# Kernel optimization log

Hardware: AMD Instinct MI355X
Metric: run time of the kernel (lower is better)

The kernel has to match this reference:

```python
import jax, jax.numpy as jnp
import numpy as np

B, S, D = 32, 2048, 128


def setup_inputs() -> dict:
    key = jax.random.key(0)
    kq, kk, kv, km = jax.random.split(key, 4)
    queries = jax.random.normal(kq, (B, S, D), dtype=jnp.float32)
    keys = jax.random.normal(kk, (B, S, D), dtype=jnp.float32)
    values = jax.random.normal(kv, (B, S, D), dtype=jnp.float32)
    attention_mask = jax.random.randint(km, (B, S, S), 0, 2, dtype=jnp.int32)
    return {"queries": queries, "keys": keys, "values": values,
            "attention_mask": attention_mask}


def reference(queries, keys, values, attention_mask):
    d = queries.shape[-1]
    # scores: [B, S, S]
    scores = jnp.einsum("bqd,bkd->bqk", queries, keys) / jnp.sqrt(
        jnp.asarray(d, queries.dtype))
    scores = jnp.where(attention_mask == 0, jnp.asarray(-1e6, scores.dtype), scores)
    attn = jax.nn.softmax(scores, axis=-1)
    # dropout prob is 0.0 (eval-equivalent), so no dropout applied
    return jnp.einsum("bqk,bkd->bqd", attn, values)
```

## Files before the change

kernel.cpp:

```cpp
#include <hip/hip_runtime.h>

#define B_ 32
#define S_ 2048
#define D_ 128

typedef __bf16 bf16;
typedef __attribute__((ext_vector_type(8))) __bf16 bf16x8;
typedef __attribute__((ext_vector_type(16))) float f32x16;

__device__ __forceinline__ f32x16 mfma32(bf16x8 a, bf16x8 b, f32x16 c) {
  return __builtin_amdgcn_mfma_f32_32x32x16_bf16(a, b, c, 0, 0, 0);
}

__device__ __forceinline__ unsigned pk2(bf16 a, bf16 b) {
  unsigned short ua = __builtin_bit_cast(unsigned short, a);
  unsigned short ub = __builtin_bit_cast(unsigned short, b);
  return (unsigned)ua | ((unsigned)ub << 16);
}

__global__ __launch_bounds__(256) void vt_prepass(const float* __restrict__ V,
                                                  bf16* __restrict__ vthi,
                                                  bf16* __restrict__ vtlo) {
  const int bid = blockIdx.x;
  const int b = bid >> 5;
  const int kt = bid & 31;
  const int kbase = kt * 64;
  const int t = threadIdx.x;

  __shared__ __align__(16) bf16 Thi[128][66];
  __shared__ __align__(16) bf16 Tlo[128][66];

  {
    const int dc = t & 31;
    const int kr0 = t >> 5;
#pragma unroll
    for (int i = 0; i < 8; ++i) {
      const int kr = kr0 + i * 8;
      const float* src = V + ((size_t)b * S_ + kbase + kr) * D_ + dc * 4;
      float4 v = *(const float4*)src;
      float f[4] = {v.x, v.y, v.z, v.w};
#pragma unroll
      for (int j = 0; j < 4; ++j) {
        bf16 hi = (bf16)f[j];
        Thi[dc * 4 + j][kr] = hi;
        Tlo[dc * 4 + j][kr] = (bf16)(f[j] - (float)hi);
      }
    }
  }
  __syncthreads();
  {
    const int d = t >> 1;
    const int part = t & 1;
    const bf16(*Tp)[66] = part ? Tlo : Thi;
    bf16* dst = part ? vtlo : vthi;
    const unsigned* row = (const unsigned*)(&Tp[d][0]);
    unsigned wbuf[32];
#pragma unroll
    for (int i = 0; i < 32; ++i) wbuf[i] = row[i];
    const size_t rowbase = ((size_t)b * D_ + d) * S_ + kbase;
#pragma unroll
    for (int j = 0; j < 8; ++j) {
      const int jj = j ^ (d & 7);
      uint4 val;
      val.x = wbuf[4 * j + 0];
      val.y = wbuf[4 * j + 1];
      val.z = wbuf[4 * j + 2];
      val.w = wbuf[4 * j + 3];
      *(uint4*)(dst + rowbase + jj * 8) = val;
    }
  }
}

__global__ __launch_bounds__(256, 2) void attn_kernel(
    const float* __restrict__ Q, const float* __restrict__ K,
    const int* __restrict__ M, const bf16* __restrict__ vthi_g,
    const bf16* __restrict__ vtlo_g, float* __restrict__ Out) {
  extern __shared__ char smem[];
  unsigned* MaskW = (unsigned*)(smem + 65536);

  const int t = threadIdx.x;
  const int w = t >> 6;
  const int i31 = t & 31;
  const int h = (t >> 5) & 1;

  const int bid = blockIdx.x;
  const int xcd = bid & 7;
  const int slot = bid >> 3;
  const int b = xcd * 4 + (slot >> 4);
  const int qt = slot & 15;
  const int qbase = qt * 128;

  const int qrow = qbase + w * 32 + i31;
  const float* qsrc = Q + ((size_t)b * S_ + qrow) * D_;
  const float sc = 0.08838834764831843f;
  bf16x8 qh[8], ql[8];
#pragma unroll
  for (int ds = 0; ds < 8; ++ds) {
    const int d0 = ds * 16 + h * 8;
    float4 a = *(const float4*)(qsrc + d0);
    float4 c = *(const float4*)(qsrc + d0 + 4);
    float f[8] = {a.x, a.y, a.z, a.w, c.x, c.y, c.z, c.w};
#pragma unroll
    for (int e = 0; e < 8; ++e) {
      float v = f[e] * sc;
      bf16 hi = (bf16)v;
      qh[ds][e] = hi;
      ql[ds][e] = (bf16)(v - (float)hi);
    }
  }

  f32x16 acc[4];
#pragma unroll
  for (int dt = 0; dt < 4; ++dt)
#pragma unroll
    for (int e = 0; e < 16; ++e) acc[dt][e] = 0.f;
  float m_run = -3.0e38f, l_run = 0.f;

  const int qloc = w * 32 + i31;
  const unsigned qsw = (unsigned)(qloc & 15);

  for (int kt = 0; kt < 32; ++kt) {
    const int kbase = kt * 64;
    __syncthreads();

    {
      const int kr = t >> 2;
      const int db = (t & 3) * 32;
      const float* src = K + ((size_t)b * S_ + kbase + kr) * D_ + db;
      const unsigned rowb = (unsigned)kr << 8;
      const unsigned sw = (unsigned)(kr & 7) << 4;
#pragma unroll
      for (int j = 0; j < 4; ++j) {
        float4 a = *(const float4*)(src + j * 8);
        float4 c = *(const float4*)(src + j * 8 + 4);
        float f[8] = {a.x, a.y, a.z, a.w, c.x, c.y, c.z, c.w};
        bf16x8 hi8, lo8;
#pragma unroll
        for (int e = 0; e < 8; ++e) {
          bf16 hi = (bf16)f[e];
          hi8[e] = hi;
          lo8[e] = (bf16)(f[e] - (float)hi);
        }
        const unsigned off = rowb + (((unsigned)((db + 8 * j) * 2)) ^ sw);
        *(bf16x8*)(smem + off) = hi8;
        *(bf16x8*)(smem + 16384 + off) = lo8;
      }
    }
    {
      const int q = t >> 1;
      const int kb = (t & 1) * 8;
      const int* src = M + ((size_t)b * S_ + qbase + q) * S_ + kbase + kb * 4;
      const unsigned qs = (unsigned)(q & 15);
#pragma unroll
      for (int i = 0; i < 8; ++i) {
        int4 mm = *(const int4*)(src + i * 4);
        unsigned packed = (unsigned)(mm.x & 1) | ((unsigned)(mm.y & 1) << 8) |
                          ((unsigned)(mm.z & 1) << 16) |
                          ((unsigned)(mm.w & 1) << 24);
        MaskW[(unsigned)q * 16 + (((unsigned)(kb + i)) ^ qs)] = packed;
      }
    }
    {
#pragma unroll
      for (int u = 0; u < 4; ++u) {
        const int off = u * 4096 + t * 16;
        const int d = off >> 7;
        const int bk = (off >> 4) & 7;
        const size_t g = ((size_t)b * D_ + d) * S_ + kbase + bk * 8;
        *(bf16x8*)(smem + 32768 + off) = *(const bf16x8*)(vthi_g + g);
        *(bf16x8*)(smem + 49152 + off) = *(const bf16x8*)(vtlo_g + g);
      }
    }
    __syncthreads();

    f32x16 s[2];
#pragma unroll
    for (int ct = 0; ct < 2; ++ct)
#pragma unroll
      for (int e = 0; e < 16; ++e) s[ct][e] = 0.f;
#pragma unroll
    for (int ct = 0; ct < 2; ++ct) {
      const unsigned rowb = (unsigned)(ct * 32 + i31) << 8;
      const unsigned sw = (unsigned)(i31 & 7) << 4;
#pragma unroll
      for (int ds = 0; ds < 8; ++ds) {
        const unsigned off = rowb + (((unsigned)(ds * 32 + h * 16)) ^ sw);
        bf16x8 kh = *(const bf16x8*)(smem + off);
        bf16x8 kl = *(const bf16x8*)(smem + 16384 + off);
        s[ct] = mfma32(kh, qh[ds], s[ct]);
        s[ct] = mfma32(kl, qh[ds], s[ct]);
        s[ct] = mfma32(kh, ql[ds], s[ct]);
      }
    }

#pragma unroll
    for (int ct = 0; ct < 2; ++ct) {
#pragma unroll
      for (int rr = 0; rr < 4; ++rr) {
        const unsigned k4 = (unsigned)(ct * 8 + rr * 2 + h);
        const unsigned mm = MaskW[(unsigned)qloc * 16 + (k4 ^ qsw)];
#pragma unroll
        for (int rb = 0; rb < 4; ++rb) {
          const int r = rr * 4 + rb;
          s[ct][r] = ((mm >> (rb * 8)) & 1u) ? s[ct][r] : -1.0e6f;
        }
      }
    }

    float mx = -3.0e38f;
#pragma unroll
    for (int ct = 0; ct < 2; ++ct)
#pragma unroll
      for (int r = 0; r < 16; ++r) mx = fmaxf(mx, s[ct][r]);
    mx = fmaxf(mx, __shfl_xor(mx, 32, 64));
    const float m_new = fmaxf(m_run, mx);
    const float alpha = __expf(m_run - m_new);
    float rs = 0.f;
#pragma unroll
    for (int ct = 0; ct < 2; ++ct)
#pragma unroll
      for (int r = 0; r < 16; ++r) {
        const float p = __expf(s[ct][r] - m_new);
        s[ct][r] = p;
        rs += p;
      }
    rs += __shfl_xor(rs, 32, 64);
    l_run = l_run * alpha + rs;
    m_run = m_new;
#pragma unroll
    for (int dt = 0; dt < 4; ++dt) acc[dt] = acc[dt] * alpha;

#pragma unroll
    for (int ks = 0; ks < 4; ++ks) {
      const int ct = ks >> 1;
      const int a0 = (ks & 1) * 8;
      unsigned PKh[4], PKl[4];
#pragma unroll
      for (int y = 0; y < 4; ++y) {
        const float p0 = s[ct][a0 + 2 * y];
        const float p1 = s[ct][a0 + 2 * y + 1];
        bf16 h0 = (bf16)p0, h1 = (bf16)p1;
        PKh[y] = pk2(h0, h1);
        PKl[y] = pk2((bf16)(p0 - (float)h0), (bf16)(p1 - (float)h1));
      }
      const unsigned s0h = h ? PKh[0] : PKh[2];
      const unsigned s1h = h ? PKh[1] : PKh[3];
      const unsigned s0l = h ? PKl[0] : PKl[2];
      const unsigned s1l = h ? PKl[1] : PKl[3];
      const unsigned r0h = __shfl_xor(s0h, 32, 64);
      const unsigned r1h = __shfl_xor(s1h, 32, 64);
      const unsigned r0l = __shfl_xor(s0l, 32, 64);
      const unsigned r1l = __shfl_xor(s1l, 32, 64);
      uint4 fh, fl;
      fh.x = h ? r0h : PKh[0];
      fh.y = h ? r1h : PKh[1];
      fh.z = h ? PKh[2] : r0h;
      fh.w = h ? PKh[3] : r1h;
      fl.x = h ? r0l : PKl[0];
      fl.y = h ? r1l : PKl[1];
      fl.z = h ? PKl[2] : r0l;
      fl.w = h ? PKl[3] : r1l;
      bf16x8 pah = __builtin_bit_cast(bf16x8, fh);
      bf16x8 pal = __builtin_bit_cast(bf16x8, fl);
#pragma unroll
      for (int dt = 0; dt < 4; ++dt) {
        const unsigned d = (unsigned)(dt * 32 + i31);
        const unsigned off = d * 128 + ((((unsigned)(ks * 2 + h)) ^ (d & 7)) * 16);
        bf16x8 vh = *(const bf16x8*)(smem + 32768 + off);
        bf16x8 vl = *(const bf16x8*)(smem + 49152 + off);
        acc[dt] = mfma32(vh, pah, acc[dt]);
        acc[dt] = mfma32(vh, pal, acc[dt]);
        acc[dt] = mfma32(vl, pah, acc[dt]);
      }
    }
  }

  const float inv_l = 1.0f / l_run;
  float* orow = Out + ((size_t)b * S_ + qbase + w * 32 + i31) * D_;
#pragma unroll
  for (int dt = 0; dt < 4; ++dt) {
#pragma unroll
    for (int rr = 0; rr < 4; ++rr) {
      float4 o;
      o.x = acc[dt][rr * 4 + 0] * inv_l;
      o.y = acc[dt][rr * 4 + 1] * inv_l;
      o.z = acc[dt][rr * 4 + 2] * inv_l;
      o.w = acc[dt][rr * 4 + 3] * inv_l;
      *(float4*)(orow + dt * 32 + rr * 8 + h * 4) = o;
    }
  }
}

extern "C" void kernel_launch(void* const* d_in, const int* in_sizes, int n_in,
                              void* d_out, int out_size, void* d_ws,
                              size_t ws_size, hipStream_t stream) {
  (void)in_sizes; (void)n_in; (void)out_size; (void)ws_size;
  const float* Q = (const float*)d_in[0];
  const float* K = (const float*)d_in[1];
  const float* V = (const float*)d_in[2];
  const int* M = (const int*)d_in[3];
  float* Out = (float*)d_out;

  bf16* vthi = (bf16*)d_ws;
  bf16* vtlo = vthi + (size_t)B_ * D_ * S_;

  static int attr_set = 0;
  if (!attr_set) {
    hipFuncSetAttribute((const void*)attn_kernel,
                        hipFuncAttributeMaxDynamicSharedMemorySize, 73728);
    attr_set = 1;
  }

  vt_prepass<<<dim3(B_ * (S_ / 64)), dim3(256), 0, stream>>>(V, vthi, vtlo);
  attn_kernel<<<dim3(512), dim3(256), 73728, stream>>>(Q, K, M, vthi, vtlo, Out);
}
```

Before: 991.5 us.

## Double-buffer K/V tiles, prepack mask to bits, 256-row query blocks with exp2

Adds a separate mask_pack kernel that turns the int32 mask into 64-bit ballot words, so the attention kernel reads one u64 per row per tile instead of streaming int4 mask data. The attention kernel now uses 512 threads with 256 query rows per block and double-buffers K and V in 128KB of LDS, prefetching the next tile into registers while computing the current one. It also folds log2(e) into the Q scale and uses exp2, applies the mask by zeroing p after the exponent, and raises wave priority around the MFMA sections. The V prepass writes a tile-contiguous layout through a packed hi/lo LDS transpose. Costs include an extra kernel launch, larger LDS and register use, and a change in semantics for fully masked rows (l=0 instead of a uniform softmax).

```diff
diff --git a/kernel.cpp b/kernel.cpp
--- a/kernel.cpp
+++ b/kernel.cpp
@@ -3,8 +3,12 @@
 #define B_ 32
 #define S_ 2048
 #define D_ 128
+#define NT 32
+#define QB 256
 
 typedef __bf16 bf16;
+typedef unsigned u32;
+typedef unsigned long long u64;
 typedef __attribute__((ext_vector_type(8))) __bf16 bf16x8;
 typedef __attribute__((ext_vector_type(16))) float f32x16;
 
@@ -12,100 +16,142 @@
   return __builtin_amdgcn_mfma_f32_32x32x16_bf16(a, b, c, 0, 0, 0);
 }
 
-__device__ __forceinline__ unsigned pk2(bf16 a, bf16 b) {
+__device__ __forceinline__ u32 pk2(bf16 a, bf16 b) {
   unsigned short ua = __builtin_bit_cast(unsigned short, a);
   unsigned short ub = __builtin_bit_cast(unsigned short, b);
-  return (unsigned)ua | ((unsigned)ub << 16);
+  return (u32)ua | ((u32)ub << 16);
 }
 
 __global__ __launch_bounds__(256) void vt_prepass(const float* __restrict__ V,
                                                   bf16* __restrict__ vthi,
                                                   bf16* __restrict__ vtlo) {
   const int bid = blockIdx.x;
-  const int b = bid >> 5;
-  const int kt = bid & 31;
+  const int b = bid >> 5, kt = bid & 31;
   const int kbase = kt * 64;
   const int t = threadIdx.x;
-
-  __shared__ __align__(16) bf16 Thi[128][66];
-  __shared__ __align__(16) bf16 Tlo[128][66];
+  __shared__ u32 Tpk[128][67];
 
   {
-    const int dc = t & 31;
-    const int kr0 = t >> 5;
+    const int dc = t & 31, kr0 = t >> 5;
 #pragma unroll
     for (int i = 0; i < 8; ++i) {
       const int kr = kr0 + i * 8;
-      const float* src = V + ((size_t)b * S_ + kbase + kr) * D_ + dc * 4;
-      float4 v = *(const float4*)src;
+      float4 v = *(const float4*)(V + ((size_t)b * S_ + kbase + kr) * D_ + dc * 4);
       float f[4] = {v.x, v.y, v.z, v.w};
 #pragma unroll
       for (int j = 0; j < 4; ++j) {
         bf16 hi = (bf16)f[j];
-        Thi[dc * 4 + j][kr] = hi;
-        Tlo[dc * 4 + j][kr] = (bf16)(f[j] - (float)hi);
+        bf16 lo = (bf16)(f[j] - (float)hi);
+        Tpk[dc * 4 + j][kr] = pk2(hi, lo);
       }
     }
   }
   __syncthreads();
-  {
-    const int d = t >> 1;
-    const int part = t & 1;
-    const bf16(*Tp)[66] = part ? Tlo : Thi;
-    bf16* dst = part ? vtlo : vthi;
-    const unsigned* row = (const unsigned*)(&Tp[d][0]);
-    unsigned wbuf[32];
-#pragma unroll
-    for (int i = 0; i < 32; ++i) wbuf[i] = row[i];
-    const size_t rowbase = ((size_t)b * D_ + d) * S_ + kbase;
-#pragma unroll
-    for (int j = 0; j < 8; ++j) {
-      const int jj = j ^ (d & 7);
-      uint4 val;
-      val.x = wbuf[4 * j + 0];
-      val.y = wbuf[4 * j + 1];
-      val.z = wbuf[4 * j + 2];
-      val.w = wbuf[4 * j + 3];
-      *(uint4*)(dst + rowbase + jj * 8) = val;
-    }
-  }
-}
-
-__global__ __launch_bounds__(256, 2) void attn_kernel(
+#pragma unroll
+  for (int p = 0; p < 4; ++p) {
+    const int g = p * 256 + t;
+    const int d = g >> 3, c = g & 7;
+    const int cs = c ^ (d & 7);
+    u32 wv[8];
+#pragma unroll
+    for (int e = 0; e < 8; ++e) wv[e] = Tpk[d][cs * 8 + e];
+    uint4 hi4, lo4;
+    u32* hp = (u32*)&hi4;
+    u32* lp = (u32*)&lo4;
+#pragma unroll
+    for (int j = 0; j < 4; ++j) {
+      hp[j] = (wv[2 * j] & 0xffffu) | (wv[2 * j + 1] << 16);
+      lp[j] = (wv[2 * j] >> 16) | (wv[2 * j + 1] & 0xffff0000u);
+    }
+    const size_t base = ((size_t)(b * NT + kt) * 128 + d) * 64 + c * 8;
+    *(uint4*)(vthi + base) = hi4;
+    *(uint4*)(vtlo + base) = lo4;
+  }
+}
+
+__global__ __launch_bounds__(256) void mask_pack(const int* __restrict__ M,
+                                                 u64* __restrict__ bits) {
+  const int wv = threadIdx.x >> 6;
+  const int lane = threadIdx.x & 63;
+  const size_t gw = (size_t)blockIdx.x * 4 + wv;
+#pragma unroll 1
+  for (int i = 0; i < 16; ++i) {
+    const size_t r = gw * 16 + i;
+    const int* src = M + r * S_;
+    u64* dst = bits + r * NT;
+#pragma unroll 1
+    for (int c = 0; c < NT; c += 8) {
+      u64 bm[8];
+#pragma unroll
+      for (int j = 0; j < 8; ++j) {
+        const int v = src[(c + j) * 64 + lane];
+        bm[j] = __ballot(v != 0);
+      }
+      if (lane == 0) {
+#pragma unroll
+        for (int j = 0; j < 8; ++j) dst[c + j] = bm[j];
+      }
+    }
+  }
+}
+
+__device__ __forceinline__ void k_convert_write(const float4 (&ka)[4], char* kdst,
+                                                int t) {
+  const int kr = t >> 3;
+  float f[16] = {ka[0].x, ka[0].y, ka[0].z, ka[0].w, ka[1].x, ka[1].y,
+                 ka[1].z, ka[1].w, ka[2].x, ka[2].y, ka[2].z, ka[2].w,
+                 ka[3].x, ka[3].y, ka[3].z, ka[3].w};
+  bf16x8 h8[2], l8[2];
+#pragma unroll
+  for (int q = 0; q < 2; ++q)
+#pragma unroll
+    for (int e = 0; e < 8; ++e) {
+      float v = f[q * 8 + e];
+      bf16 hi = (bf16)v;
+      h8[q][e] = hi;
+      l8[q][e] = (bf16)(v - (float)hi);
+    }
+  const u32 blk = (u32)(t & 7) * 2, swz = (u32)(kr & 7);
+#pragma unroll
+  for (int q = 0; q < 2; ++q) {
+    const u32 off = (u32)kr * 256 + (((blk + q) ^ swz) * 16);
+    *(bf16x8*)(kdst + off) = h8[q];
+    *(bf16x8*)(kdst + 16384 + off) = l8[q];
+  }
+}
+
+__global__ __launch_bounds__(512, 2) void attn_kernel(
     const float* __restrict__ Q, const float* __restrict__ K,
-    const int* __restrict__ M, const bf16* __restrict__ vthi_g,
+    const u64* __restrict__ MB, const bf16* __restrict__ vthi_g,
     const bf16* __restrict__ vtlo_g, float* __restrict__ Out) {
   extern __shared__ char smem[];
-  unsigned* MaskW = (unsigned*)(smem + 65536);
-
   const int t = threadIdx.x;
   const int w = t >> 6;
   const int i31 = t & 31;
   const int h = (t >> 5) & 1;
 
   const int bid = blockIdx.x;
-  const int xcd = bid & 7;
-  const int slot = bid >> 3;
-  const int b = xcd * 4 + (slot >> 4);
-  const int qt = slot & 15;
-  const int qbase = qt * 128;
-
-  const int qrow = qbase + w * 32 + i31;
-  const float* qsrc = Q + ((size_t)b * S_ + qrow) * D_;
-  const float sc = 0.08838834764831843f;
+  const int b = (bid & 7) * 4 + ((bid >> 3) >> 3);
+  const int qbase = ((bid >> 3) & 7) * QB;
+  const int qloc = w * 32 + i31;
+
+  const float sc = 0.08838834764831843f * 1.4426950408889634f;
   bf16x8 qh[8], ql[8];
-#pragma unroll
-  for (int ds = 0; ds < 8; ++ds) {
-    const int d0 = ds * 16 + h * 8;
-    float4 a = *(const float4*)(qsrc + d0);
-    float4 c = *(const float4*)(qsrc + d0 + 4);
-    float f[8] = {a.x, a.y, a.z, a.w, c.x, c.y, c.z, c.w};
-#pragma unroll
-    for (int e = 0; e < 8; ++e) {
-      float v = f[e] * sc;
-      bf16 hi = (bf16)v;
-      qh[ds][e] = hi;
-      ql[ds][e] = (bf16)(v - (float)hi);
+  {
+    const float* qsrc = Q + ((size_t)b * S_ + qbase + qloc) * D_;
+#pragma unroll
+    for (int ds = 0; ds < 8; ++ds) {
+      const int d0 = ds * 16 + h * 8;
+      float4 a = *(const float4*)(qsrc + d0);
+      float4 c = *(const float4*)(qsrc + d0 + 4);
+      float f[8] = {a.x, a.y, a.z, a.w, c.x, c.y, c.z, c.w};
+#pragma unroll
+      for (int e = 0; e < 8; ++e) {
+        float v = f[e] * sc;
+        bf16 hi = (bf16)v;
+        qh[ds][e] = hi;
+        ql[ds][e] = (bf16)(v - (float)hi);
+      }
     }
   }
 
@@ -116,96 +162,73 @@
     for (int e = 0; e < 16; ++e) acc[dt][e] = 0.f;
   float m_run = -3.0e38f, l_run = 0.f;
 
-  const int qloc = w * 32 + i31;
-  const unsigned qsw = (unsigned)(qloc & 15);
-
-  for (int kt = 0; kt < 32; ++kt) {
-    const int kbase = kt * 64;
-    __syncthreads();
-
-    {
-      const int kr = t >> 2;
-      const int db = (t & 3) * 32;
-      const float* src = K + ((size_t)b * S_ + kbase + kr) * D_ + db;
-      const unsigned rowb = (unsigned)kr << 8;
-      const unsigned sw = (unsigned)(kr & 7) << 4;
-#pragma unroll
-      for (int j = 0; j < 4; ++j) {
-        float4 a = *(const float4*)(src + j * 8);
-        float4 c = *(const float4*)(src + j * 8 + 4);
-        float f[8] = {a.x, a.y, a.z, a.w, c.x, c.y, c.z, c.w};
-        bf16x8 hi8, lo8;
-#pragma unroll
-        for (int e = 0; e < 8; ++e) {
-          bf16 hi = (bf16)f[e];
-          hi8[e] = hi;
-          lo8[e] = (bf16)(f[e] - (float)hi);
-        }
-        const unsigned off = rowb + (((unsigned)((db + 8 * j) * 2)) ^ sw);
-        *(bf16x8*)(smem + off) = hi8;
-        *(bf16x8*)(smem + 16384 + off) = lo8;
-      }
-    }
-    {
-      const int q = t >> 1;
-      const int kb = (t & 1) * 8;
-      const int* src = M + ((size_t)b * S_ + qbase + q) * S_ + kbase + kb * 4;
-      const unsigned qs = (unsigned)(q & 15);
-#pragma unroll
-      for (int i = 0; i < 8; ++i) {
-        int4 mm = *(const int4*)(src + i * 4);
-        unsigned packed = (unsigned)(mm.x & 1) | ((unsigned)(mm.y & 1) << 8) |
-                          ((unsigned)(mm.z & 1) << 16) |
-                          ((unsigned)(mm.w & 1) << 24);
-        MaskW[(unsigned)q * 16 + (((unsigned)(kb + i)) ^ qs)] = packed;
-      }
-    }
-    {
-#pragma unroll
-      for (int u = 0; u < 4; ++u) {
-        const int off = u * 4096 + t * 16;
-        const int d = off >> 7;
-        const int bk = (off >> 4) & 7;
-        const size_t g = ((size_t)b * D_ + d) * S_ + kbase + bk * 8;
-        *(bf16x8*)(smem + 32768 + off) = *(const bf16x8*)(vthi_g + g);
-        *(bf16x8*)(smem + 49152 + off) = *(const bf16x8*)(vtlo_g + g);
-      }
-    }
-    __syncthreads();
+  const float* kbat = K + (size_t)b * S_ * D_;
+  const bf16* vh_b = vthi_g + (size_t)b * NT * 8192;
+  const bf16* vl_b = vtlo_g + (size_t)b * NT * 8192;
+  const u64* mrow = MB + ((size_t)b * S_ + qbase + qloc) * NT;
+
+  const int kr = t >> 3;
+  const int kcol = (t & 7) * 16;
+
+  u64 mcur = mrow[0];
+  {
+    float4 ka[4];
+    const float* ks = kbat + (size_t)kr * D_ + kcol;
+#pragma unroll
+    for (int j = 0; j < 4; ++j) ka[j] = *(const float4*)(ks + j * 4);
+    uint4 vr0 = *(const uint4*)(vh_b + (size_t)t * 8);
+    uint4 vr1 = *(const uint4*)(vh_b + (size_t)(512 + t) * 8);
+    uint4 vr2 = *(const uint4*)(vl_b + (size_t)t * 8);
+    uint4 vr3 = *(const uint4*)(vl_b + (size_t)(512 + t) * 8);
+    k_convert_write(ka, smem, t);
+    char* vb = smem + 32768;
+    *(uint4*)(vb + t * 16) = vr0;
+    *(uint4*)(vb + (512 + t) * 16) = vr1;
+    *(uint4*)(vb + 16384 + t * 16) = vr2;
+    *(uint4*)(vb + 16384 + (512 + t) * 16) = vr3;
+  }
+  __syncthreads();
+
+  for (int kt = 0; kt < NT; ++kt) {
+    const int cb = kt & 1;
+    const char* kb = smem + cb * 65536;
+    const bool pre = (kt + 1 < NT);
+    float4 ka[4];
+    uint4 vr0, vr1, vr2, vr3;
+    u64 mnxt = 0;
+    if (pre) {
+      const float* ks = kbat + (size_t)(kt + 1) * 64 * D_ + (size_t)kr * D_ + kcol;
+#pragma unroll
+      for (int j = 0; j < 4; ++j) ka[j] = *(const float4*)(ks + j * 4);
+      const size_t tb = (size_t)(kt + 1) * 8192;
+      vr0 = *(const uint4*)(vh_b + tb + (size_t)t * 8);
+      vr1 = *(const uint4*)(vh_b + tb + (size_t)(512 + t) * 8);
+      vr2 = *(const uint4*)(vl_b + tb + (size_t)t * 8);
+      vr3 = *(const uint4*)(vl_b + tb + (size_t)(512 + t) * 8);
+      mnxt = mrow[kt + 1];
+    }
 
     f32x16 s[2];
 #pragma unroll
     for (int ct = 0; ct < 2; ++ct)
 #pragma unroll
       for (int e = 0; e < 16; ++e) s[ct][e] = 0.f;
+    __builtin_amdgcn_s_setprio(1);
 #pragma unroll
     for (int ct = 0; ct < 2; ++ct) {
-      const unsigned rowb = (unsigned)(ct * 32 + i31) << 8;
-      const unsigned sw = (unsigned)(i31 & 7) << 4;
+      const u32 rowb = (u32)(ct * 32 + i31) * 256;
+      const u32 sw = (u32)(i31 & 7) << 4;
 #pragma unroll
       for (int ds = 0; ds < 8; ++ds) {
-        const unsigned off = rowb + (((unsigned)(ds * 32 + h * 16)) ^ sw);
-        bf16x8 kh = *(const bf16x8*)(smem + off);
-        bf16x8 kl = *(const bf16x8*)(smem + 16384 + off);
+        const u32 off = rowb + (((u32)(ds * 32 + h * 16)) ^ sw);
+        bf16x8 kh = *(const bf16x8*)(kb + off);
+        bf16x8 kl = *(const bf16x8*)(kb + 16384 + off);
         s[ct] = mfma32(kh, qh[ds], s[ct]);
         s[ct] = mfma32(kl, qh[ds], s[ct]);
         s[ct] = mfma32(kh, ql[ds], s[ct]);
       }
     }
-
-#pragma unroll
-    for (int ct = 0; ct < 2; ++ct) {
-#pragma unroll
-      for (int rr = 0; rr < 4; ++rr) {
-        const unsigned k4 = (unsigned)(ct * 8 + rr * 2 + h);
-        const unsigned mm = MaskW[(unsigned)qloc * 16 + (k4 ^ qsw)];
-#pragma unroll
-        for (int rb = 0; rb < 4; ++rb) {
-          const int r = rr * 4 + rb;
-          s[ct][r] = ((mm >> (rb * 8)) & 1u) ? s[ct][r] : -1.0e6f;
-        }
-      }
-    }
+    __builtin_amdgcn_s_setprio(0);
 
     float mx = -3.0e38f;
 #pragma unroll
@@ -214,27 +237,34 @@
       for (int r = 0; r < 16; ++r) mx = fmaxf(mx, s[ct][r]);
     mx = fmaxf(mx, __shfl_xor(mx, 32, 64));
     const float m_new = fmaxf(m_run, mx);
-    const float alpha = __expf(m_run - m_new);
+    const float alpha = exp2f(m_run - m_new);
+    const u32 mw0 = (u32)mcur, mw1 = (u32)(mcur >> 32);
     float rs = 0.f;
 #pragma unroll
-    for (int ct = 0; ct < 2; ++ct)
+    for (int ct = 0; ct < 2; ++ct) {
+      const u32 mword = ct ? mw1 : mw0;
 #pragma unroll
       for (int r = 0; r < 16; ++r) {
-        const float p = __expf(s[ct][r] - m_new);
+        const int pos = (r & 3) + 8 * (r >> 2) + 4 * h;
+        float p = exp2f(s[ct][r] - m_new);
+        p = ((mword >> pos) & 1u) ? p : 0.f;
         s[ct][r] = p;
         rs += p;
       }
+    }
     rs += __shfl_xor(rs, 32, 64);
     l_run = l_run * alpha + rs;
     m_run = m_new;
 #pragma unroll
     for (int dt = 0; dt < 4; ++dt) acc[dt] = acc[dt] * alpha;
 
+    const char* vbc = kb + 32768;
+    __builtin_amdgcn_s_setprio(1);
 #pragma unroll
     for (int ks = 0; ks < 4; ++ks) {
       const int ct = ks >> 1;
       const int a0 = (ks & 1) * 8;
-      unsigned PKh[4], PKl[4];
+      u32 PKh[4], PKl[4];
 #pragma unroll
       for (int y = 0; y < 4; ++y) {
         const float p0 = s[ct][a0 + 2 * y];
@@ -243,14 +273,14 @@
         PKh[y] = pk2(h0, h1);
         PKl[y] = pk2((bf16)(p0 - (float)h0), (bf16)(p1 - (float)h1));
       }
-      const unsigned s0h = h ? PKh[0] : PKh[2];
-      const unsigned s1h = h ? PKh[1] : PKh[3];
-      const unsigned s0l = h ? PKl[0] : PKl[2];
-      const unsigned s1l = h ? PKl[1] : PKl[3];
-      const unsigned r0h = __shfl_xor(s0h, 32, 64);
-      const unsigned r1h = __shfl_xor(s1h, 32, 64);
-      const unsigned r0l = __shfl_xor(s0l, 32, 64);
-      const unsigned r1l = __shfl_xor(s1l, 32, 64);
+      const u32 s0h = h ? PKh[0] : PKh[2];
+      const u32 s1h = h ? PKh[1] : PKh[3];
+      const u32 s0l = h ? PKl[0] : PKl[2];
+      const u32 s1l = h ? PKl[1] : PKl[3];
+      const u32 r0h = __shfl_xor(s0h, 32, 64);
+      const u32 r1h = __shfl_xor(s1h, 32, 64);
+      const u32 r0l = __shfl_xor(s0l, 32, 64);
+      const u32 r1l = __shfl_xor(s1l, 32, 64);
       uint4 fh, fl;
       fh.x = h ? r0h : PKh[0];
       fh.y = h ? r1h : PKh[1];
@@ -264,19 +294,32 @@
       bf16x8 pal = __builtin_bit_cast(bf16x8, fl);
 #pragma unroll
       for (int dt = 0; dt < 4; ++dt) {
-        const unsigned d = (unsigned)(dt * 32 + i31);
-        const unsigned off = d * 128 + ((((unsigned)(ks * 2 + h)) ^ (d & 7)) * 16);
-        bf16x8 vh = *(const bf16x8*)(smem + 32768 + off);
-        bf16x8 vl = *(const bf16x8*)(smem + 49152 + off);
+        const u32 d = (u32)(dt * 32 + i31);
+        const u32 off = d * 128 + ((((u32)(ks * 2 + h)) ^ (d & 7)) * 16);
+        bf16x8 vh = *(const bf16x8*)(vbc + off);
+        bf16x8 vl = *(const bf16x8*)(vbc + 16384 + off);
         acc[dt] = mfma32(vh, pah, acc[dt]);
         acc[dt] = mfma32(vh, pal, acc[dt]);
         acc[dt] = mfma32(vl, pah, acc[dt]);
       }
     }
+    __builtin_amdgcn_s_setprio(0);
+
+    if (pre) {
+      char* kdst = smem + (cb ^ 1) * 65536;
+      k_convert_write(ka, kdst, t);
+      char* vb = kdst + 32768;
+      *(uint4*)(vb + t * 16) = vr0;
+      *(uint4*)(vb + (512 + t) * 16) = vr1;
+      *(uint4*)(vb + 16384 + t * 16) = vr2;
+      *(uint4*)(vb + 16384 + (512 + t) * 16) = vr3;
+    }
+    __syncthreads();
+    mcur = mnxt;
   }
 
   const float inv_l = 1.0f / l_run;
-  float* orow = Out + ((size_t)b * S_ + qbase + w * 32 + i31) * D_;
+  float* orow = Out + ((size_t)b * S_ + qbase + qloc) * D_;
 #pragma unroll
   for (int dt = 0; dt < 4; ++dt) {
 #pragma unroll
@@ -301,16 +344,20 @@
   const int* M = (const int*)d_in[3];
   float* Out = (float*)d_out;
 
+  const size_t vt_el = (size_t)B_ * S_ * D_;
   bf16* vthi = (bf16*)d_ws;
-  bf16* vtlo = vthi + (size_t)B_ * D_ * S_;
+  bf16* vtlo = vthi + vt_el;
+  u64* mbits = (u64*)(vtlo + vt_el);
 
   static int attr_set = 0;
   if (!attr_set) {
     hipFuncSetAttribute((const void*)attn_kernel,
-                        hipFuncAttributeMaxDynamicSharedMemorySize, 73728);
+                        hipFuncAttributeMaxDynamicSharedMemorySize, 131072);
     attr_set = 1;
   }
 
-  vt_prepass<<<dim3(B_ * (S_ / 64)), dim3(256), 0, stream>>>(V, vthi, vtlo);
-  attn_kernel<<<dim3(512), dim3(256), 73728, stream>>>(Q, K, M, vthi, vtlo, Out);
-}
+  vt_prepass<<<dim3(B_ * NT), dim3(256), 0, stream>>>(V, vthi, vtlo);
+  mask_pack<<<dim3(1024), dim3(256), 0, stream>>>(M, mbits);
+  attn_kernel<<<dim3(256), dim3(512), 131072, stream>>>(Q, K, mbits, vthi, vtlo,
+                                                        Out);
+}
```

After: 957.9 us. -3.4%, faster.
